# Kernel tuning notes

Hardware: AMD Instinct MI355X
Metric: run time of the kernel (lower is better)

## Reference

```python
import jax, jax.numpy as jnp
import numpy as np

D, N, K, NC = 768, 128, 25, 3          # d_model, n_spins, K_mc_eval, n_classes
GAMMA, T_MF, DAMPING = 0.25, 25, 0.7   # mean-field Ising constants from config


def _layernorm(x, g, b):
    m = x.mean(-1, keepdims=True)
    v = ((x - m) ** 2).mean(-1, keepdims=True)
    return (x - m) / jnp.sqrt(v + 1e-5) * g + b


def setup_inputs() -> dict:
    key = jax.random.key(0)
    ks = jax.random.split(key, 16)
    B, S = 256, 128
    return {
        'hidden_states': jax.random.normal(ks[0], (B, S, D), jnp.float32),
        'coalitions': (jax.random.uniform(ks[1], (K, N)) < 0.5).astype(jnp.float32),
        'W_v': jax.random.normal(ks[2], (D, D), jnp.float32) * 0.02,
        'scale': jnp.ones((1,), jnp.float32) * 0.1,
        'local_field': jax.random.normal(ks[3], (N,), jnp.float32) * 0.1,
        'J': jax.random.normal(ks[4], (N, N), jnp.float32) * (0.1 / np.sqrt(N)),
        'Wp': jax.random.normal(ks[5], (D, N), jnp.float32) * 0.02,
        'bp': jnp.zeros((N,), jnp.float32),
        'W1': jax.random.normal(ks[6], (N, 256), jnp.float32) * 0.02,
        'b1': jnp.zeros((256,), jnp.float32),
        'g1': jnp.ones((256,), jnp.float32),
        'be1': jnp.zeros((256,), jnp.float32),
        'W2': jax.random.normal(ks[7], (256, 128), jnp.float32) * 0.02,
        'b2': jnp.zeros((128,), jnp.float32),
        'g2': jnp.ones((128,), jnp.float32),
        'be2': jnp.zeros((128,), jnp.float32),
        'W3': jax.random.normal(ks[8], (128, NC), jnp.float32) * 0.02,
        'b3': jnp.zeros((NC,), jnp.float32),
    }


def reference(hidden_states, coalitions, W_v, scale, local_field, J, Wp, bp,
              W1, b1, g1, be1, W2, b2, g2, be2, W3, b3):
    # --- game theory: all K coalition values in one batched pass ----------
    # coalition_value(f, c) = relu(scale * || sum_n c_n f_n W_v ||).
    # Masking then summing is linear in the mask, so contract mask first.
    feats = hidden_states[:, :N, :]                       # [B, N, D]
    cs = jnp.einsum('kn,bnd->bkd', coalitions, feats)     # [B, K, D]
    proj = jnp.einsum('bkd,de->bke', cs, W_v)             # [B, K, D]
    v = jax.nn.relu(jnp.linalg.norm(proj, axis=-1) * scale[0])  # [B, K]
    # Monte-Carlo Shapley: mean(v | spin i in coalition) - mean(v | not in)
    cnt1 = coalitions.sum(0)                              # [N]
    cnt0 = K - cnt1
    sum_w = v @ coalitions                                # [B, N]
    sum_wo = v.sum(1, keepdims=True) - sum_w
    valid = (cnt1 > 0) & (cnt0 > 0)
    shapley = jnp.where(valid,
                        sum_w / jnp.maximum(cnt1, 1.0) - sum_wo / jnp.maximum(cnt0, 1.0),
                        0.0)                              # [B, N]
    # --- mean-field Ising on projected CLS features -----------------------
    pooled = hidden_states[:, 0, :]                       # [B, D] (CLS)
    m0 = jnp.tanh((pooled @ Wp + bp) * 0.1)               # [B, N]
    Jm = J * (1.0 - jnp.eye(N, dtype=J.dtype))            # zero diagonal

    def step(m, _):
        h = local_field + m @ Jm
        new = jnp.tanh(h / GAMMA)
        return DAMPING * new + (1.0 - DAMPING) * m, None

    m, _ = jax.lax.scan(step, m0, None, length=T_MF)
    h_fin = local_field + m @ Jm
    # log(2*cosh(x)) == logaddexp(x, -x), numerically stable
    free_energy = -GAMMA * jnp.sum(jnp.logaddexp(h_fin / GAMMA, -h_fin / GAMMA),
                                   axis=-1, keepdims=True)   # [B, 1]
    # --- classifier head on expected spins --------------------------------
    x = jax.nn.gelu(_layernorm(m @ W1 + b1, g1, be1), approximate=False)
    x = jax.nn.gelu(_layernorm(x @ W2 + b2, g2, be2), approximate=False)
    logits = x @ W3 + b3                                   # [B, NC]
    return logits, free_energy, shapley
```

## Files before the change

kernel.cpp:

```cpp
#include <hip/hip_runtime.h>
#include <math.h>


typedef _Float16 h8 __attribute__((ext_vector_type(8)));
typedef float f4v __attribute__((ext_vector_type(4)));

constexpr int Bq = 256, Dq = 768, Nq = 128, Kq = 25;
constexpr size_t WVT_OFF  = 0;
constexpr size_t CS_OFF   = 1179648;
constexpr size_t PART_OFF = 11010048;
constexpr size_t M0_OFF   = 11112448;

template <int KS>
__device__ __forceinline__ void ldb24(const float* __restrict__ hb2, float* arr) {
  #pragma unroll
  for (int ct = 0; ct < 3; ++ct) {
    const float* hp = hb2 + (size_t)(KS * 32) * 768 + ct * 16;
    #pragma unroll
    for (int j = 0; j < 8; ++j) arr[ct * 8 + j] = hp[(size_t)j * 768];
  }
}

__device__ __forceinline__ void stepk(const float* arr, const h8& a0, const h8& a1,
                                      f4v acc[2][3]) {
  #pragma unroll
  for (int ct = 0; ct < 3; ++ct) {
    h8 bfv;
    #pragma unroll
    for (int j = 0; j < 8; ++j) bfv[j] = (_Float16)arr[ct * 8 + j];
    acc[0][ct] = __builtin_amdgcn_mfma_f32_16x16x32_f16(a0, bfv, acc[0][ct], 0, 0, 0);
    acc[1][ct] = __builtin_amdgcn_mfma_f32_16x16x32_f16(a1, bfv, acc[1][ct], 0, 0, 0);
  }
}

__global__ __launch_bounds__(256, 2) void k1_front(const float* __restrict__ hst,
                                                   const float* __restrict__ coal,
                                                   const float* __restrict__ Wv,
                                                   const float* __restrict__ Wp,
                                                   const float* __restrict__ bp,
                                                   _Float16* __restrict__ wvt,
                                                   _Float16* __restrict__ csf,
                                                   float* __restrict__ m0g) {
  __shared__ float tile[32 * 33];
  __shared__ float part2[256];
  const int t = threadIdx.x;
  const int b = blockIdx.x & 255;
  const int cc = blockIdx.x >> 8;
  const int l = t & 63, w = t >> 6;
  const int colbase = cc * 192;
  const int kb = (l >> 4) * 8;
  const float* hb = hst + (size_t)b * (128 * 768);

  if (blockIdx.x < 576) {
    const int bx = blockIdx.x % 24, by = blockIdx.x / 24;
    const int r = t >> 3, c4 = (t & 7) * 4;
    const float4 v = *reinterpret_cast<const float4*>(Wv + (size_t)(by * 32 + r) * 768 + bx * 32 + c4);
    tile[r * 33 + c4 + 0] = v.x; tile[r * 33 + c4 + 1] = v.y;
    tile[r * 33 + c4 + 2] = v.z; tile[r * 33 + c4 + 3] = v.w;
    __syncthreads();
    _Float16* dp = wvt + (size_t)(bx * 32 + r) * 768 + by * 32 + c4;
    dp[0] = (_Float16)tile[(c4 + 0) * 33 + r];
    dp[1] = (_Float16)tile[(c4 + 1) * 33 + r];
    dp[2] = (_Float16)tile[(c4 + 2) * 33 + r];
    dp[3] = (_Float16)tile[(c4 + 3) * 33 + r];
  }

  h8 afrag[2][4];
  #pragma unroll
  for (int Mt = 0; Mt < 2; ++Mt) {
    const int row = Mt * 16 + (l & 15);
    #pragma unroll
    for (int ks = 0; ks < 4; ++ks) {
      h8 v;
      if (row < 25) {
        const float4 p0 = *reinterpret_cast<const float4*>(coal + row * 128 + ks * 32 + kb);
        const float4 p1 = *reinterpret_cast<const float4*>(coal + row * 128 + ks * 32 + kb + 4);
        v[0] = (_Float16)p0.x; v[1] = (_Float16)p0.y;
        v[2] = (_Float16)p0.z; v[3] = (_Float16)p0.w;
        v[4] = (_Float16)p1.x; v[5] = (_Float16)p1.y;
        v[6] = (_Float16)p1.z; v[7] = (_Float16)p1.w;
      } else {
        #pragma unroll
        for (int j = 0; j < 8; ++j) v[j] = (_Float16)0.f;
      }
      afrag[Mt][ks] = v;
    }
  }

  f4v acc[2][3];
  #pragma unroll
  for (int Mt = 0; Mt < 2; ++Mt)
    #pragma unroll
    for (int ct = 0; ct < 3; ++ct) acc[Mt][ct] = (f4v){0.f, 0.f, 0.f, 0.f};

  const float* hb2 = hb + (size_t)kb * 768 + colbase + w * 48 + (l & 15);
  float ta[24], tb[24];
  ldb24<0>(hb2, ta);
  ldb24<1>(hb2, tb);
  stepk(ta, afrag[0][0], afrag[1][0], acc);
  ldb24<2>(hb2, ta);
  stepk(tb, afrag[0][1], afrag[1][1], acc);
  ldb24<3>(hb2, tb);
  stepk(ta, afrag[0][2], afrag[1][2], acc);
  stepk(tb, afrag[0][3], afrag[1][3], acc);

  #pragma unroll
  for (int Mt = 0; Mt < 2; ++Mt) {
    const int row0 = Mt * 16 + (l >> 4) * 4;
    #pragma unroll
    for (int ct = 0; ct < 3; ++ct) {
      const int col = colbase + (w * 3 + ct) * 16 + (l & 15);
      #pragma unroll
      for (int r = 0; r < 4; ++r) {
        const int rr = row0 + r;
        if (rr < 25)
          csf[((size_t)b * 25 + rr) * 768 + col] = (_Float16)acc[Mt][ct][r];
      }
    }
  }

  if (cc == 0) {
    const int j = t & 127, sg = t >> 7;
    float s = 0.f;
    for (int d = sg * 384; d < sg * 384 + 384; d += 4) {
      const float4 p4 = *reinterpret_cast<const float4*>(hb + d);
      s += p4.x * Wp[(d + 0) * 128 + j] + p4.y * Wp[(d + 1) * 128 + j]
         + p4.z * Wp[(d + 2) * 128 + j] + p4.w * Wp[(d + 3) * 128 + j];
    }
    part2[t] = s;
    __syncthreads();
    if (t < 128) {
      const float a0 = bp[t] + part2[t] + part2[t + 128];
      m0g[b * 128 + t] = tanhf(a0 * 0.1f);
    }
  }
}

__device__ __forceinline__ float bsum4(float v, float* red) {
  #pragma unroll
  for (int o = 32; o > 0; o >>= 1) v += __shfl_down(v, o, 64);
  __syncthreads();
  if ((threadIdx.x & 63) == 0) red[threadIdx.x >> 6] = v;
  __syncthreads();
  return red[0] + red[1] + red[2] + red[3];
}

__global__ __launch_bounds__(512, 1) void k23(
    const _Float16* __restrict__ csA, const _Float16* __restrict__ wvtB,
    float* __restrict__ part,
    const float* __restrict__ Jg,   const float* __restrict__ lf,
    const float* __restrict__ m0g,
    const float* __restrict__ W1, const float* __restrict__ b1,
    const float* __restrict__ g1, const float* __restrict__ be1,
    const float* __restrict__ W2, const float* __restrict__ b2,
    const float* __restrict__ g2, const float* __restrict__ be2,
    const float* __restrict__ W3, const float* __restrict__ b3,
    float* __restrict__ out) {
  __shared__ __align__(16) char lds[(128 + 192) * 64];
  __shared__ __align__(16) float m_sh[128];
  __shared__ float pmf[256];
  __shared__ __align__(16) float x1[256];
  __shared__ float x2[128];
  __shared__ float red[8];
  const int tid = threadIdx.x;

  if (blockIdx.x < 200) {
    char* ldsA = lds;
    char* ldsB = lds + 8192;
    const int l = tid & 63, w = tid >> 6;
    const int rg = blockIdx.x >> 2, cc = blockIdx.x & 3;
    const size_t rowbase = (size_t)rg * 128;
    const int colbase = cc * 192;
    const int wm = w & 1, wn = w >> 1;

    const int fch = ((l >> 4) ^ (((l & 15) >> 1) & 3)) * 16;
    const int aoff = (l & 15) * 64 + fch;
    const int boff = (l & 15) * 64 + fch;

    const int srow = tid >> 2, sich = tid & 3;
    const int sch = sich ^ ((srow >> 1) & 3);
    const size_t gA_base = (rowbase + srow) * 768 + sich * 8;
    const size_t gB0_base = (size_t)(colbase + srow) * 768 + sich * 8;
    const size_t gB1_base = (size_t)(colbase + 128 + srow) * 768 + sich * 8;
    char* ldsA_w = ldsA + srow * 64 + sch * 16;
    char* ldsB0_w = ldsB + srow * 64 + sch * 16;
    char* ldsB1_w = ldsB + (128 + srow) * 64 + sch * 16;

    f4v acc[4][3];
    #pragma unroll
    for (int mt = 0; mt < 4; ++mt)
      #pragma unroll
      for (int nt = 0; nt < 3; ++nt) acc[mt][nt] = (f4v){0.f, 0.f, 0.f, 0.f};

    uint4 ra = *reinterpret_cast<const uint4*>(csA + gA_base);
    uint4 rb0 = *reinterpret_cast<const uint4*>(wvtB + gB0_base);
    uint4 rb1 = {0, 0, 0, 0};
    if (tid < 256) rb1 = *reinterpret_cast<const uint4*>(wvtB + gB1_base);

    for (int ks = 0; ks < 24; ++ks) {
      *reinterpret_cast<uint4*>(ldsA_w) = ra;
      *reinterpret_cast<uint4*>(ldsB0_w) = rb0;
      if (tid < 256) *reinterpret_cast<uint4*>(ldsB1_w) = rb1;
      if (ks < 23) {
        ra = *reinterpret_cast<const uint4*>(csA + gA_base + (ks + 1) * 32);
        rb0 = *reinterpret_cast<const uint4*>(wvtB + gB0_base + (ks + 1) * 32);
        if (tid < 256) rb1 = *reinterpret_cast<const uint4*>(wvtB + gB1_base + (ks + 1) * 32);
      }
      __syncthreads();
      h8 af[4];
      #pragma unroll
      for (int mt = 0; mt < 4; ++mt)
        af[mt] = *reinterpret_cast<const h8*>(ldsA + (wm * 4 + mt) * 1024 + aoff);
      #pragma unroll
      for (int nt = 0; nt < 3; ++nt) {
        const h8 bf = *reinterpret_cast<const h8*>(ldsB + (wn * 3 + nt) * 1024 + boff);
        #pragma unroll
        for (int mt = 0; mt < 4; ++mt)
          acc[mt][nt] = __builtin_amdgcn_mfma_f32_16x16x32_f16(af[mt], bf, acc[mt][nt], 0, 0, 0);
      }
      __syncthreads();
    }

    float* redw = reinterpret_cast<float*>(lds);
    #pragma unroll
    for (int mt = 0; mt < 4; ++mt) {
      #pragma unroll
      for (int r = 0; r < 4; ++r) {
        float s = acc[mt][0][r] * acc[mt][0][r] + acc[mt][1][r] * acc[mt][1][r]
                + acc[mt][2][r] * acc[mt][2][r];
        s += __shfl_xor(s, 1); s += __shfl_xor(s, 2);
        s += __shfl_xor(s, 4); s += __shfl_xor(s, 8);
        if ((l & 15) == 0) {
          const int row_local = (wm * 4 + mt) * 16 + (l >> 4) * 4 + r;
          redw[row_local * 4 + wn] = s;
        }
      }
    }
    __syncthreads();
    if (tid < 128) {
      const float tot = redw[tid * 4 + 0] + redw[tid * 4 + 1]
                      + redw[tid * 4 + 2] + redw[tid * 4 + 3];
      part[(size_t)cc * 6400 + rowbase + tid] = tot;
    }
  } else {
    const int t = tid;
    const int b = blockIdx.x - 200;
    const int tn = t & 127, th = t >> 7;

    float Jreg[64];
    if (t < 256) {
      #pragma unroll
      for (int i = 0; i < 64; ++i)
        Jreg[i] = Jg[(size_t)(th * 64 + i) * 128 + tn];
    }

    float mloc = 0.f, lfv = 0.f, Jdg = 0.f;
    if (t < 128) {
      mloc = m0g[b * 128 + t];
      m_sh[t] = mloc;
      lfv = lf[t];
      Jdg = Jg[t * 128 + t];
    }
    __syncthreads();

    float hs = 0.f;
    for (int it = 0; it <= 25; ++it) {
      if (t < 256) {
        float ps0 = 0.f, ps1 = 0.f, ps2 = 0.f, ps3 = 0.f;
        #pragma unroll
        for (int q = 0; q < 16; ++q) {
          const float4 m4 = *reinterpret_cast<const float4*>(m_sh + th * 64 + q * 4);
          ps0 += Jreg[q * 4 + 0] * m4.x;
          ps1 += Jreg[q * 4 + 1] * m4.y;
          ps2 += Jreg[q * 4 + 2] * m4.z;
          ps3 += Jreg[q * 4 + 3] * m4.w;
        }
        pmf[t] = (ps0 + ps1) + (ps2 + ps3);
      }
      __syncthreads();
      if (it < 25) {
        if (t < 128) {
          const float h = lfv - mloc * Jdg + pmf[t] + pmf[t + 128];
          mloc = 0.7f * tanhf(h * 4.0f) + 0.3f * mloc;
          m_sh[t] = mloc;
        }
        __syncthreads();
      } else {
        if (t < 128) hs = lfv - mloc * Jdg + pmf[t] + pmf[t + 128];
      }
    }

    {
      const float a2 = (t < 128) ? fabsf(hs * 4.0f) : 0.f;
      const float fe = (t < 128) ? (a2 + log1pf(expf(-2.f * a2))) : 0.f;
      const float tot = bsum4(fe, red);
      if (t == 0) out[768 + b] = -0.25f * tot;
    }

    float u = 0.f;
    if (t < 256) {
      u = b1[t];
      #pragma unroll 4
      for (int n = 0; n < 128; n += 4) {
        const float4 m4 = *reinterpret_cast<const float4*>(m_sh + n);
        u += m4.x * W1[(n + 0) * 256 + t] + m4.y * W1[(n + 1) * 256 + t]
           + m4.z * W1[(n + 2) * 256 + t] + m4.w * W1[(n + 3) * 256 + t];
      }
    }
    const float mean1 = bsum4(t < 256 ? u : 0.f, red) * (1.f / 256.f);
    const float xm1 = u - mean1;
    const float var1 = bsum4(t < 256 ? xm1 * xm1 : 0.f, red) * (1.f / 256.f);
    if (t < 256) {
      const float xln1 = xm1 * rsqrtf(var1 + 1e-5f) * g1[t] + be1[t];
      x1[t] = 0.5f * xln1 * (1.f + erff(xln1 * 0.70710678118654752f));
    }
    __syncthreads();

    float u2 = 0.f;
    if (t < 128) {
      u2 = b2[t];
      #pragma unroll 4
      for (int n = 0; n < 256; n += 4) {
        const float4 x4 = *reinterpret_cast<const float4*>(x1 + n);
        u2 += x4.x * W2[(n + 0) * 128 + t] + x4.y * W2[(n + 1) * 128 + t]
            + x4.z * W2[(n + 2) * 128 + t] + x4.w * W2[(n + 3) * 128 + t];
      }
    }
    const float mean2 = bsum4(t < 128 ? u2 : 0.f, red) * (1.f / 128.f);
    const float xm2 = u2 - mean2;
    const float var2 = bsum4(t < 128 ? xm2 * xm2 : 0.f, red) * (1.f / 128.f);
    if (t < 128) {
      const float xln2 = xm2 * rsqrtf(var2 + 1e-5f) * g2[t] + be2[t];
      x2[t] = 0.5f * xln2 * (1.f + erff(xln2 * 0.70710678118654752f));
    }
    __syncthreads();

    if (t < 3) {
      float lg = b3[t];
      #pragma unroll 4
      for (int n = 0; n < 128; ++n) lg += x2[n] * W3[n * 3 + t];
      out[b * 3 + t] = lg;
    }
  }
}

__global__ __launch_bounds__(128, 1) void k3b(const float* __restrict__ part,
                                              const float* __restrict__ coal,
                                              const float* __restrict__ scale,
                                              float* __restrict__ out) {
  __shared__ float vsh[32];
  const int t = threadIdx.x, b = blockIdx.x;
  if (t < 25) {
    const float sq = part[b * 25 + t] + part[6400 + b * 25 + t]
                   + part[12800 + b * 25 + t] + part[19200 + b * 25 + t];
    vsh[t] = fmaxf(sqrtf(sq) * scale[0], 0.f);
  }
  __syncthreads();
  float sw = 0.f, c1 = 0.f, vs = 0.f;
  #pragma unroll
  for (int k = 0; k < 25; ++k) {
    const float c = coal[k * 128 + t];
    const float vk = vsh[k];
    sw += c * vk; vs += vk; c1 += c;
  }
  const float c0 = 25.f - c1;
  float shap = 0.f;
  if (c1 > 0.5f && c0 > 0.5f)
    shap = sw / fmaxf(c1, 1.f) - (vs - sw) / fmaxf(c0, 1.f);
  out[1024 + b * 128 + t] = shap;
}

extern "C" void kernel_launch(void* const* d_in, const int* in_sizes, int n_in,
                              void* d_out, int out_size, void* d_ws, size_t ws_size,
                              hipStream_t stream) {
  const float* hst   = (const float*)d_in[0];
  const float* coal  = (const float*)d_in[1];
  const float* Wv    = (const float*)d_in[2];
  const float* scale = (const float*)d_in[3];
  const float* lf    = (const float*)d_in[4];
  const float* Jg    = (const float*)d_in[5];
  const float* Wp    = (const float*)d_in[6];
  const float* bp    = (const float*)d_in[7];
  const float* W1    = (const float*)d_in[8];
  const float* b1    = (const float*)d_in[9];
  const float* g1    = (const float*)d_in[10];
  const float* be1   = (const float*)d_in[11];
  const float* W2    = (const float*)d_in[12];
  const float* b2    = (const float*)d_in[13];
  const float* g2    = (const float*)d_in[14];
  const float* be2   = (const float*)d_in[15];
  const float* W3    = (const float*)d_in[16];
  const float* b3    = (const float*)d_in[17];
  float* out = (float*)d_out;

  char* ws = (char*)d_ws;
  _Float16* wvt = (_Float16*)(ws + WVT_OFF);
  _Float16* csf = (_Float16*)(ws + CS_OFF);
  float* part   = (float*)(ws + PART_OFF);
  float* m0g    = (float*)(ws + M0_OFF);

  hipLaunchKernelGGL(k1_front, dim3(1024), dim3(256), 0, stream,
                     hst, coal, Wv, Wp, bp, wvt, csf, m0g);
  hipLaunchKernelGGL(k23, dim3(456), dim3(512), 0, stream,
                     csf, wvt, part, Jg, lf, m0g,
                     W1, b1, g1, be1, W2, b2, g2, be2, W3, b3, out);
  hipLaunchKernelGGL(k3b, dim3(256), dim3(128), 0, stream,
                     part, coal, scale, out);
}
```

Measured before the change: 69.20 us.

## Double-buffer mean-field spins to halve barriers; manually unroll GEMM k-loop by two

The mean-field iteration now uses 128 threads, each holding a full J column in 128 registers, and ping-pongs between two shared spin buffers. This removes the partial-sum exchange and cuts the barriers per iteration from two to one. The GEMM branch is unrolled by two, keeping two sets of prefetch registers so global loads run two k-steps ahead. The cost is halving the threads doing the matvec and higher register pressure, 128 floats of J plus extra prefetch registers, which risks spills under the 512-thread launch bound.

```diff
diff --git a/kernel.cpp b/kernel.cpp
--- a/kernel.cpp
+++ b/kernel.cpp
@@ -145,6 +145,27 @@
   return red[0] + red[1] + red[2] + red[3];
 }
 
+__device__ __forceinline__ void mfstep(const float* __restrict__ src,
+                                       float* __restrict__ dst,
+                                       const float* Jreg, float& mloc,
+                                       float lfv, float Jdg, int t) {
+  if (t < 128) {
+    float p0 = 0.f, p1 = 0.f, p2 = 0.f, p3 = 0.f;
+    #pragma unroll
+    for (int q = 0; q < 32; ++q) {
+      const float4 m4 = *reinterpret_cast<const float4*>(src + q * 4);
+      p0 += Jreg[q * 4 + 0] * m4.x;
+      p1 += Jreg[q * 4 + 1] * m4.y;
+      p2 += Jreg[q * 4 + 2] * m4.z;
+      p3 += Jreg[q * 4 + 3] * m4.w;
+    }
+    const float h = lfv - mloc * Jdg + ((p0 + p1) + (p2 + p3));
+    mloc = 0.7f * tanhf(h * 4.0f) + 0.3f * mloc;
+    dst[t] = mloc;
+  }
+  __syncthreads();
+}
+
 __global__ __launch_bounds__(512, 1) void k23(
     const _Float16* __restrict__ csA, const _Float16* __restrict__ wvtB,
     float* __restrict__ part,
@@ -157,8 +178,8 @@
     const float* __restrict__ W3, const float* __restrict__ b3,
     float* __restrict__ out) {
   __shared__ __align__(16) char lds[(128 + 192) * 64];
-  __shared__ __align__(16) float m_sh[128];
-  __shared__ float pmf[256];
+  __shared__ __align__(16) float m_shA[128];
+  __shared__ __align__(16) float m_shB[128];
   __shared__ __align__(16) float x1[256];
   __shared__ float x2[128];
   __shared__ float red[8];
@@ -192,31 +213,60 @@
       #pragma unroll
       for (int nt = 0; nt < 3; ++nt) acc[mt][nt] = (f4v){0.f, 0.f, 0.f, 0.f};
 
-    uint4 ra = *reinterpret_cast<const uint4*>(csA + gA_base);
-    uint4 rb0 = *reinterpret_cast<const uint4*>(wvtB + gB0_base);
-    uint4 rb1 = {0, 0, 0, 0};
-    if (tid < 256) rb1 = *reinterpret_cast<const uint4*>(wvtB + gB1_base);
-
-    for (int ks = 0; ks < 24; ++ks) {
-      *reinterpret_cast<uint4*>(ldsA_w) = ra;
-      *reinterpret_cast<uint4*>(ldsB0_w) = rb0;
-      if (tid < 256) *reinterpret_cast<uint4*>(ldsB1_w) = rb1;
-      if (ks < 23) {
-        ra = *reinterpret_cast<const uint4*>(csA + gA_base + (ks + 1) * 32);
-        rb0 = *reinterpret_cast<const uint4*>(wvtB + gB0_base + (ks + 1) * 32);
-        if (tid < 256) rb1 = *reinterpret_cast<const uint4*>(wvtB + gB1_base + (ks + 1) * 32);
+    uint4 raA = *reinterpret_cast<const uint4*>(csA + gA_base);
+    uint4 rb0A = *reinterpret_cast<const uint4*>(wvtB + gB0_base);
+    uint4 rb1A = {0, 0, 0, 0};
+    if (tid < 256) rb1A = *reinterpret_cast<const uint4*>(wvtB + gB1_base);
+    uint4 raB = *reinterpret_cast<const uint4*>(csA + gA_base + 32);
+    uint4 rb0B = *reinterpret_cast<const uint4*>(wvtB + gB0_base + 32);
+    uint4 rb1B = {0, 0, 0, 0};
+    if (tid < 256) rb1B = *reinterpret_cast<const uint4*>(wvtB + gB1_base + 32);
+
+    for (int kp = 0; kp < 12; ++kp) {
+      *reinterpret_cast<uint4*>(ldsA_w) = raA;
+      *reinterpret_cast<uint4*>(ldsB0_w) = rb0A;
+      if (tid < 256) *reinterpret_cast<uint4*>(ldsB1_w) = rb1A;
+      if (kp < 11) {
+        raA = *reinterpret_cast<const uint4*>(csA + gA_base + (2 * kp + 2) * 32);
+        rb0A = *reinterpret_cast<const uint4*>(wvtB + gB0_base + (2 * kp + 2) * 32);
+        if (tid < 256) rb1A = *reinterpret_cast<const uint4*>(wvtB + gB1_base + (2 * kp + 2) * 32);
       }
       __syncthreads();
-      h8 af[4];
-      #pragma unroll
-      for (int mt = 0; mt < 4; ++mt)
-        af[mt] = *reinterpret_cast<const h8*>(ldsA + (wm * 4 + mt) * 1024 + aoff);
-      #pragma unroll
-      for (int nt = 0; nt < 3; ++nt) {
-        const h8 bf = *reinterpret_cast<const h8*>(ldsB + (wn * 3 + nt) * 1024 + boff);
+      {
+        h8 af[4];
         #pragma unroll
         for (int mt = 0; mt < 4; ++mt)
-          acc[mt][nt] = __builtin_amdgcn_mfma_f32_16x16x32_f16(af[mt], bf, acc[mt][nt], 0, 0, 0);
+          af[mt] = *reinterpret_cast<const h8*>(ldsA + (wm * 4 + mt) * 1024 + aoff);
+        #pragma unroll
+        for (int nt = 0; nt < 3; ++nt) {
+          const h8 bf = *reinterpret_cast<const h8*>(ldsB + (wn * 3 + nt) * 1024 + boff);
+          #pragma unroll
+          for (int mt = 0; mt < 4; ++mt)
+            acc[mt][nt] = __builtin_amdgcn_mfma_f32_16x16x32_f16(af[mt], bf, acc[mt][nt], 0, 0, 0);
+        }
+      }
+      __syncthreads();
+      *reinterpret_cast<uint4*>(ldsA_w) = raB;
+      *reinterpret_cast<uint4*>(ldsB0_w) = rb0B;
+      if (tid < 256) *reinterpret_cast<uint4*>(ldsB1_w) = rb1B;
+      if (kp < 11) {
+        raB = *reinterpret_cast<const uint4*>(csA + gA_base + (2 * kp + 3) * 32);
+        rb0B = *reinterpret_cast<const uint4*>(wvtB + gB0_base + (2 * kp + 3) * 32);
+        if (tid < 256) rb1B = *reinterpret_cast<const uint4*>(wvtB + gB1_base + (2 * kp + 3) * 32);
+      }
+      __syncthreads();
+      {
+        h8 af[4];
+        #pragma unroll
+        for (int mt = 0; mt < 4; ++mt)
+          af[mt] = *reinterpret_cast<const h8*>(ldsA + (wm * 4 + mt) * 1024 + aoff);
+        #pragma unroll
+        for (int nt = 0; nt < 3; ++nt) {
+          const h8 bf = *reinterpret_cast<const h8*>(ldsB + (wn * 3 + nt) * 1024 + boff);
+          #pragma unroll
+          for (int mt = 0; mt < 4; ++mt)
+            acc[mt][nt] = __builtin_amdgcn_mfma_f32_16x16x32_f16(af[mt], bf, acc[mt][nt], 0, 0, 0);
+        }
       }
       __syncthreads();
     }
@@ -245,49 +295,42 @@
   } else {
     const int t = tid;
     const int b = blockIdx.x - 200;
-    const int tn = t & 127, th = t >> 7;
-
-    float Jreg[64];
-    if (t < 256) {
+
+    float Jreg[128];
+    if (t < 128) {
       #pragma unroll
-      for (int i = 0; i < 64; ++i)
-        Jreg[i] = Jg[(size_t)(th * 64 + i) * 128 + tn];
+      for (int i = 0; i < 128; ++i)
+        Jreg[i] = Jg[(size_t)i * 128 + t];
     }
 
     float mloc = 0.f, lfv = 0.f, Jdg = 0.f;
     if (t < 128) {
       mloc = m0g[b * 128 + t];
-      m_sh[t] = mloc;
+      m_shA[t] = mloc;
       lfv = lf[t];
       Jdg = Jg[t * 128 + t];
     }
     __syncthreads();
 
+    #pragma unroll 1
+    for (int p = 0; p < 12; ++p) {
+      mfstep(m_shA, m_shB, Jreg, mloc, lfv, Jdg, t);
+      mfstep(m_shB, m_shA, Jreg, mloc, lfv, Jdg, t);
+    }
+    mfstep(m_shA, m_shB, Jreg, mloc, lfv, Jdg, t);
+
     float hs = 0.f;
-    for (int it = 0; it <= 25; ++it) {
-      if (t < 256) {
-        float ps0 = 0.f, ps1 = 0.f, ps2 = 0.f, ps3 = 0.f;
-        #pragma unroll
-        for (int q = 0; q < 16; ++q) {
-          const float4 m4 = *reinterpret_cast<const float4*>(m_sh + th * 64 + q * 4);
-          ps0 += Jreg[q * 4 + 0] * m4.x;
-          ps1 += Jreg[q * 4 + 1] * m4.y;
-          ps2 += Jreg[q * 4 + 2] * m4.z;
-          ps3 += Jreg[q * 4 + 3] * m4.w;
-        }
-        pmf[t] = (ps0 + ps1) + (ps2 + ps3);
-      }
-      __syncthreads();
-      if (it < 25) {
-        if (t < 128) {
-          const float h = lfv - mloc * Jdg + pmf[t] + pmf[t + 128];
-          mloc = 0.7f * tanhf(h * 4.0f) + 0.3f * mloc;
-          m_sh[t] = mloc;
-        }
-        __syncthreads();
-      } else {
-        if (t < 128) hs = lfv - mloc * Jdg + pmf[t] + pmf[t + 128];
-      }
+    if (t < 128) {
+      float p0 = 0.f, p1 = 0.f, p2 = 0.f, p3 = 0.f;
+      #pragma unroll
+      for (int q = 0; q < 32; ++q) {
+        const float4 m4 = *reinterpret_cast<const float4*>(m_shB + q * 4);
+        p0 += Jreg[q * 4 + 0] * m4.x;
+        p1 += Jreg[q * 4 + 1] * m4.y;
+        p2 += Jreg[q * 4 + 2] * m4.z;
+        p3 += Jreg[q * 4 + 3] * m4.w;
+      }
+      hs = lfv - mloc * Jdg + ((p0 + p1) + (p2 + p3));
     }
 
     {
@@ -302,7 +345,7 @@
       u = b1[t];
       #pragma unroll 4
       for (int n = 0; n < 128; n += 4) {
-        const float4 m4 = *reinterpret_cast<const float4*>(m_sh + n);
+        const float4 m4 = *reinterpret_cast<const float4*>(m_shB + n);
         u += m4.x * W1[(n + 0) * 256 + t] + m4.y * W1[(n + 1) * 256 + t]
            + m4.z * W1[(n + 2) * 256 + t] + m4.w * W1[(n + 3) * 256 + t];
       }
```

Measured after the change: 80.00 us. 15.6% more time.
